# Kernel optimization log

Measured on AMD Instinct MI355X. Metric: run time of the kernel, lower is better.

## Reference

```python
import jax, jax.numpy as jnp
import numpy as np

N, I, C, P, K = 16, 4096, 16, 16, 8
NI = N * I
E_RAND = 524288
CP = C + P


def setup_inputs() -> dict:
    key = jax.random.key(0)
    ks = jax.random.split(key, 14)
    x = jax.random.normal(ks[0], (N, I, C), dtype=jnp.float32)
    # random edges (stand-in for data-dependent kmeans complete subgraphs) + self loops
    src = jax.random.randint(ks[1], (E_RAND,), 0, NI)
    dst = jax.random.randint(ks[2], (E_RAND,), 0, NI)
    loops = jnp.arange(NI)
    edge_index = jnp.stack([jnp.concatenate([src, loops]),
                            jnp.concatenate([dst, loops])], axis=0)  # [2, E]
    # cluster labels: point p of cloud n -> cluster (p % K) + n*K, every cluster non-empty
    cluster_index = (jnp.arange(NI) % K) + (jnp.arange(NI) // I) * K
    sC = 1.0 / np.sqrt(C)
    sCP = 1.0 / np.sqrt(CP)
    return {
        "x": x,
        "edge_index": edge_index,
        "cluster_index": cluster_index,
        "F_W": jax.random.normal(ks[3], (C, C * CP), dtype=jnp.float32) * sC,
        "F_b": jnp.zeros((C * CP,), dtype=jnp.float32),
        "W_W": jax.random.normal(ks[4], (C, C * CP), dtype=jnp.float32) * sC,
        "W_b": jnp.zeros((C * CP,), dtype=jnp.float32),
        "M_W": jax.random.normal(ks[5], (CP, 1), dtype=jnp.float32) * sCP,
        "M_b": jnp.zeros((1,), dtype=jnp.float32),
        "B": jax.random.normal(ks[6], (CP,), dtype=jnp.float32),
        "mlp1_W": jax.random.normal(ks[7], (CP, CP), dtype=jnp.float32) * sCP,
        "mlp1_b": jnp.zeros((CP,), dtype=jnp.float32),
        "mlp2_W": jax.random.normal(ks[8], (CP, CP), dtype=jnp.float32) * sCP,
        "mlp2_b": jnp.zeros((CP,), dtype=jnp.float32),
        "sc_W": jax.random.normal(ks[9], (CP, CP), dtype=jnp.float32) * sCP,
        "sc_b": jnp.zeros((CP,), dtype=jnp.float32),
        "lr": jnp.asarray(1.0, dtype=jnp.float32),
    }


def _shrinking_unit(x, edge_index, cluster_index,
                    F_W, F_b, W_W, W_b, M_W, M_b, B,
                    mlp1_W, mlp1_b, mlp2_W, mlp2_b, sc_W, sc_b, lr):
    xf = x.reshape(-1, C)                      # [NI, C]
    src, dst = edge_index[0], edge_index[1]    # message flows src(j) -> dst(i)
    x_i = xf[dst]                              # [E, C]
    x_j = xf[src]
    # message: per-edge transform matrix F(x_j - x_i) in R^{(C+P) x C} applied to x_i
    msg = ((x_j - x_i) @ F_W + F_b).reshape(-1, CP, C)   # [E, CP, C]
    msg = jnp.einsum('epc,ec->ep', msg, x_i)             # [E, CP]
    # mean aggregation over incoming edges (self-loops guarantee deg >= 1)
    deg = jax.ops.segment_sum(jnp.ones_like(dst, dtype=x.dtype), dst, num_segments=NI)
    aggr = jax.ops.segment_sum(msg, dst, num_segments=NI) / deg[:, None]   # [NI, CP]
    # update
    weight = aggr @ M_W + M_b                             # [NI, 1]
    aggr = aggr * weight
    transform = (xf @ W_W + W_b).reshape(-1, CP, C)       # [NI, CP, C]
    aggr = aggr + jnp.einsum('npc,nc->np', transform, xf)
    conv = jax.nn.sigmoid(aggr + B).reshape(N, I, CP)     # [N, I, CP]
    # Aggregation module: pad x to CP, squeeze-excite style softmax gate
    x_pad = jnp.pad(x, ((0, 0), (0, 0), (0, P)))          # [N, I, CP]
    S1 = jnp.mean(x_pad, axis=1)                          # [N, CP]
    S2 = jnp.mean(conv, axis=1)
    Z1 = S1 @ mlp1_W + mlp1_b
    Z2 = S2 @ mlp2_W + mlp2_b
    M = jax.nn.softmax(jnp.stack([Z1, Z2], axis=0), axis=0)  # [2, N, CP]
    fused = M[0][:, None, :] * x_pad + M[1][:, None, :] * conv  # [N, I, CP]
    # MaxPool over clusters
    pooled = jax.ops.segment_max(fused.reshape(-1, CP), cluster_index,
                                 num_segments=K * N).reshape(N, K, CP)
    # SelfCorrelation: residual MLP scaled by learnable lambda
    pf = pooled.reshape(-1, CP)
    out = (pf + lr * (pf @ sc_W + sc_b)).reshape(N, K, CP)
    return out


def reference(x, edge_index, cluster_index, F_W, F_b, W_W, W_b, M_W, M_b, B,
              mlp1_W, mlp1_b, mlp2_W, mlp2_b, sc_W, sc_b, lr):
    return _shrinking_unit(x, edge_index, cluster_index, F_W, F_b, W_W, W_b,
                           M_W, M_b, B, mlp1_W, mlp1_b, mlp2_W, mlp2_b,
                           sc_W, sc_b, lr)
```

## Files before the change

### kernel.cpp

```cpp
#include <hip/hip_runtime.h>
#include <hip/hip_bf16.h>


#define POOL_NBLK 32

__device__ __forceinline__ unsigned fmap(float f) {
    unsigned u = __float_as_uint(f);
    return (u & 0x80000000u) ? ~u : (u | 0x80000000u);
}
__device__ __forceinline__ float funmap(unsigned m) {
    return (m & 0x80000000u) ? __uint_as_float(m & 0x7FFFFFFFu)
                             : __uint_as_float(~m);
}

__device__ __forceinline__ void load16(const float* __restrict__ p, float* r) {
    const float4* q = (const float4*)p;
    float4 a = q[0], b = q[1], c = q[2], d = q[3];
    r[0]=a.x; r[1]=a.y; r[2]=a.z; r[3]=a.w;
    r[4]=b.x; r[5]=b.y; r[6]=b.z; r[7]=b.w;
    r[8]=c.x; r[9]=c.y; r[10]=c.z; r[11]=c.w;
    r[12]=d.x; r[13]=d.y; r[14]=d.z; r[15]=d.w;
}

__global__ __launch_bounds__(256) void edge_scatter(
    const float* __restrict__ x, const int* __restrict__ ei,
    float* __restrict__ s, float* __restrict__ deg, int E)
{
    int tid = blockIdx.x * 256 + threadIdx.x;
    int e = tid >> 4, c = tid & 15;
    if (e >= E) return;
    int src = ei[e];
    int dst = ei[E + e];
    atomicAdd(&s[(size_t)dst * 16 + c], x[(size_t)src * 16 + c]);
    if (c == 0) atomicAdd(&deg[dst], 1.0f);
}

__global__ __launch_bounds__(256) void node_update(
    const float* __restrict__ x, const float* __restrict__ s,
    const float* __restrict__ deg,
    const float* __restrict__ Fw, const float* __restrict__ Fb,
    const float* __restrict__ Ww, const float* __restrict__ Wb,
    const float* __restrict__ Mw, const float* __restrict__ Mb,
    const float* __restrict__ Bv,
    float* __restrict__ conv, float* __restrict__ S1s, float* __restrict__ S2s)
{
    __shared__ float wlds[8192];
    __shared__ float aF[256 * 17];
    const int tid = threadIdx.x;
    #pragma unroll
    for (int k = 0; k < 8192; k += 256) wlds[k + tid] = Fw[k + tid];

    const int lane = tid & 63;
    const int w4   = tid >> 6;
    const int h    = w4 & 1;
    const int i    = blockIdx.x * 128 + ((w4 >> 1) << 6) + lane;
    const int n    = i >> 12;

    float xr[16], tr[16];
    load16(x + (size_t)i * 16, xr);
    load16(s + (size_t)i * 16, tr);
    const float invd = 1.0f / deg[i];
    #pragma unroll
    for (int c = 0; c < 16; ++c) tr[c] = tr[c] * invd - xr[c];

    __syncthreads();

    const int pbase = h << 8;
    #pragma unroll 1
    for (int pp = 0; pp < 16; ++pp) {
        const int cb0 = pbase + (pp << 4);
        float acc = 0.0f;
        #pragma unroll
        for (int cb = 0; cb < 16; cb += 4) {
            float u0 = Fb[cb0+cb+0], u1 = Fb[cb0+cb+1];
            float u2 = Fb[cb0+cb+2], u3 = Fb[cb0+cb+3];
            #pragma unroll
            for (int cp = 0; cp < 16; ++cp) {
                const float4 f = *(const float4*)&wlds[(cp << 9) + cb0 + cb];
                u0 = fmaf(tr[cp], f.x, u0);
                u1 = fmaf(tr[cp], f.y, u1);
                u2 = fmaf(tr[cp], f.z, u2);
                u3 = fmaf(tr[cp], f.w, u3);
            }
            acc = fmaf(xr[cb+0], u0, acc);
            acc = fmaf(xr[cb+1], u1, acc);
            acc = fmaf(xr[cb+2], u2, acc);
            acc = fmaf(xr[cb+3], u3, acc);
        }
        aF[tid * 17 + pp] = acc;
    }
    __syncthreads();
    #pragma unroll
    for (int k = 0; k < 8192; k += 256) wlds[k + tid] = Ww[k + tid];

    float w = Mb[0];
    {
        const int base0 = (tid & ~64) * 17;
        const int base1 = base0 + 64 * 17;
        #pragma unroll
        for (int q = 0; q < 16; ++q) w = fmaf(aF[base0 + q], Mw[q], w);
        #pragma unroll
        for (int q = 0; q < 16; ++q) w = fmaf(aF[base1 + q], Mw[16 + q], w);
    }
    __syncthreads();

    #pragma unroll 1
    for (int pp = 0; pp < 16; ++pp) {
        const int cb0 = pbase + (pp << 4);
        float acc = 0.0f;
        #pragma unroll
        for (int cb = 0; cb < 16; cb += 4) {
            float u0 = Wb[cb0+cb+0], u1 = Wb[cb0+cb+1];
            float u2 = Wb[cb0+cb+2], u3 = Wb[cb0+cb+3];
            #pragma unroll
            for (int cp = 0; cp < 16; ++cp) {
                const float4 f = *(const float4*)&wlds[(cp << 9) + cb0 + cb];
                u0 = fmaf(xr[cp], f.x, u0);
                u1 = fmaf(xr[cp], f.y, u1);
                u2 = fmaf(xr[cp], f.z, u2);
                u3 = fmaf(xr[cp], f.w, u3);
            }
            acc = fmaf(xr[cb+0], u0, acc);
            acc = fmaf(xr[cb+1], u1, acc);
            acc = fmaf(xr[cb+2], u2, acc);
            acc = fmaf(xr[cb+3], u3, acc);
        }
        const float z  = aF[tid * 17 + pp] * w + acc + Bv[(h << 4) + pp];
        const float cv = 1.0f / (1.0f + expf(-z));
        conv[(size_t)i * 32 + (h << 4) + pp] = cv;
        float v = cv;
        v += __shfl_xor(v, 1);
        v += __shfl_xor(v, 2);
        v += __shfl_xor(v, 4);
        v += __shfl_xor(v, 8);
        v += __shfl_xor(v, 16);
        v += __shfl_xor(v, 32);
        if (lane == 0) atomicAdd(&S2s[n * 32 + (h << 4) + pp], v);
    }
    if (h == 0) {
        #pragma unroll
        for (int c = 0; c < 16; ++c) {
            float v = xr[c];
            v += __shfl_xor(v, 1);
            v += __shfl_xor(v, 2);
            v += __shfl_xor(v, 4);
            v += __shfl_xor(v, 8);
            v += __shfl_xor(v, 16);
            v += __shfl_xor(v, 32);
            if (lane == 0) atomicAdd(&S1s[n * 32 + c], v);
        }
    }
}

__global__ void gate_kernel(const float* __restrict__ S1s, const float* __restrict__ S2s,
    const float* __restrict__ m1W, const float* __restrict__ m1b,
    const float* __restrict__ m2W, const float* __restrict__ m2b,
    float* __restrict__ M0, float* __restrict__ M1, float invI)
{
    int t = threadIdx.x;
    int n = t >> 5, p = t & 31;
    float z1 = m1b[p], z2 = m2b[p];
    #pragma unroll
    for (int q = 0; q < 32; ++q) {
        z1 = fmaf(S1s[n * 32 + q] * invI, m1W[q * 32 + p], z1);
        z2 = fmaf(S2s[n * 32 + q] * invI, m2W[q * 32 + p], z2);
    }
    float m = fmaxf(z1, z2);
    float e1 = expf(z1 - m), e2 = expf(z2 - m);
    float inv = 1.0f / (e1 + e2);
    M0[t] = e1 * inv;
    M1[t] = e2 * inv;
}

__global__ __launch_bounds__(256) void pool_kernel(
    const float* __restrict__ x, const float* __restrict__ conv,
    const int* __restrict__ cl, const float* __restrict__ M0,
    const float* __restrict__ M1, unsigned* __restrict__ blkT,
    int NI, int nSlots)
{
    __shared__ unsigned utab[4096];
    const int tid = threadIdx.x;
    for (int t = tid; t < nSlots; t += 256) utab[t] = 0u;
    __syncthreads();

    for (int i = blockIdx.x * 256 + tid; i < NI; i += POOL_NBLK * 256) {
        int n = i >> 12;
        int c = cl[i];
        const float* m0 = M0 + n * 32;
        const float* m1 = M1 + n * 32;
        float cr[32];
        {
            const float4* q = (const float4*)(conv + (size_t)i * 32);
            #pragma unroll
            for (int b = 0; b < 8; ++b) {
                float4 v = q[b];
                cr[b*4+0] = v.x; cr[b*4+1] = v.y; cr[b*4+2] = v.z; cr[b*4+3] = v.w;
            }
        }
        float xr[16];
        load16(x + (size_t)i * 16, xr);
        unsigned* up = utab + (c << 5);
        #pragma unroll
        for (int p = 0; p < 16; ++p) {
            float f = fmaf(m0[p], xr[p], m1[p] * cr[p]);
            atomicMax(&up[p], fmap(f));
        }
        #pragma unroll
        for (int p = 16; p < 32; ++p) {
            float f = m1[p] * cr[p];
            atomicMax(&up[p], fmap(f));
        }
    }
    __syncthreads();
    unsigned* dst = blkT + (size_t)blockIdx.x * nSlots;
    for (int t = tid; t < nSlots; t += 256) dst[t] = utab[t];
}

__global__ __launch_bounds__(256) void pool_reduce(
    const unsigned* __restrict__ blkT, unsigned* __restrict__ pooledM, int nSlots)
{
    int t = blockIdx.x * 256 + threadIdx.x;
    if (t >= nSlots) return;
    unsigned m = 0u;
    #pragma unroll
    for (int b = 0; b < POOL_NBLK; ++b)
        m = max(m, blkT[(size_t)b * nSlots + t]);
    pooledM[t] = m;
}

__global__ void final_kernel(const unsigned* __restrict__ pooledM,
    const float* __restrict__ scW, const float* __restrict__ scb,
    const float* __restrict__ lr, float* __restrict__ out, int total)
{
    int t = blockIdx.x * 256 + threadIdx.x;
    if (t >= total) return;
    int g = t >> 5, p = t & 31;
    float acc = scb[p];
    float self = 0.0f;
    #pragma unroll
    for (int q = 0; q < 32; ++q) {
        float v = funmap(pooledM[g * 32 + q]);
        if (q == p) self = v;
        acc = fmaf(v, scW[q * 32 + p], acc);
    }
    out[t] = self + lr[0] * acc;
}

extern "C" void kernel_launch(void* const* d_in, const int* in_sizes, int n_in,
                              void* d_out, int out_size, void* d_ws, size_t ws_size,
                              hipStream_t stream)
{
    const float* x   = (const float*)d_in[0];
    const int*   ei  = (const int*)d_in[1];
    const int*   clus= (const int*)d_in[2];
    const float* Fw  = (const float*)d_in[3];
    const float* Fb  = (const float*)d_in[4];
    const float* Ww  = (const float*)d_in[5];
    const float* Wb  = (const float*)d_in[6];
    const float* Mw  = (const float*)d_in[7];
    const float* Mb  = (const float*)d_in[8];
    const float* Bv  = (const float*)d_in[9];
    const float* m1W = (const float*)d_in[10];
    const float* m1b = (const float*)d_in[11];
    const float* m2W = (const float*)d_in[12];
    const float* m2b = (const float*)d_in[13];
    const float* scW = (const float*)d_in[14];
    const float* scb = (const float*)d_in[15];
    const float* lr  = (const float*)d_in[16];

    const int NI = in_sizes[0] / 16;
    const int E  = in_sizes[1] / 2;
    const int nG = NI >> 12;
    const int nC = out_size / 32;
    const int nSlots = nC * 32;

    float* ws   = (float*)d_ws;
    float* s_   = ws;
    float* deg_ = s_ + (size_t)NI * 16;
    float* S1s  = deg_ + NI;
    float* S2s  = S1s + nG * 32;
    unsigned* pooledM = (unsigned*)(S2s + nG * 32);
    float* M0   = (float*)(pooledM + nSlots);
    float* M1   = M0 + nG * 32;
    float* conv = M1 + nG * 32;
    unsigned* blkT = (unsigned*)s_;

    size_t need_bytes = (size_t)((char*)(conv + (size_t)NI * 32) - (char*)ws);
    if (ws_size < need_bytes || nSlots > 4096) return;

    size_t zbytes = (size_t)((char*)(pooledM + nSlots) - (char*)ws);
    hipMemsetAsync(d_ws, 0, zbytes, stream);

    edge_scatter<<<dim3((E * 16 + 255) / 256), dim3(256), 0, stream>>>(x, ei, s_, deg_, E);
    node_update<<<dim3(NI * 2 / 256), dim3(256), 0, stream>>>(
        x, s_, deg_, Fw, Fb, Ww, Wb, Mw, Mb, Bv, conv, S1s, S2s);
    gate_kernel<<<dim3(1), dim3(nG * 32), 0, stream>>>(
        S1s, S2s, m1W, m1b, m2W, m2b, M0, M1, 1.0f / 4096.0f);
    pool_kernel<<<dim3(POOL_NBLK), dim3(256), 0, stream>>>(
        x, conv, clus, M0, M1, blkT, NI, nSlots);
    pool_reduce<<<dim3((nSlots + 255) / 256), dim3(256), 0, stream>>>(
        blkT, pooledM, nSlots);
    final_kernel<<<dim3((out_size + 255) / 256), dim3(256), 0, stream>>>(
        pooledM, scW, scb, lr, (float*)d_out, out_size);
}
```

Baseline: 276.8 us.

## Process two nodes per thread in node_update and widen pool block count

```diff
diff --git a/kernel.cpp b/kernel.cpp
--- a/kernel.cpp
+++ b/kernel.cpp
@@ -2,7 +2,7 @@
 #include <hip/hip_bf16.h>
 
 
-#define POOL_NBLK 32
+#define POOL_NBLK 256
 
 __device__ __forceinline__ unsigned fmap(float f) {
     unsigned u = __float_as_uint(f);
@@ -35,7 +35,7 @@
     if (c == 0) atomicAdd(&deg[dst], 1.0f);
 }
 
-__global__ __launch_bounds__(256) void node_update(
+__global__ __launch_bounds__(128) void node_update(
     const float* __restrict__ x, const float* __restrict__ s,
     const float* __restrict__ deg,
     const float* __restrict__ Fw, const float* __restrict__ Fb,
@@ -45,23 +45,34 @@
     float* __restrict__ conv, float* __restrict__ S1s, float* __restrict__ S2s)
 {
     __shared__ float wlds[8192];
-    __shared__ float aF[256 * 17];
+    __shared__ float aF[128 * 34];
     const int tid = threadIdx.x;
+
+    {
+        const float4* F4 = (const float4*)Fw;
+        float4* w4 = (float4*)wlds;
+        #pragma unroll
+        for (int k = 0; k < 16; ++k) w4[k * 128 + tid] = F4[k * 128 + tid];
+    }
+
+    const int lane = tid & 63;
+    const int h    = tid >> 6;
+    const int i0   = blockIdx.x * 128 + lane;
+    const int i1   = i0 + 64;
+    const int n    = i0 >> 12;
+
+    float xr0[16], tr0[16], xr1[16], tr1[16];
+    load16(x + (size_t)i0 * 16, xr0);
+    load16(s + (size_t)i0 * 16, tr0);
+    load16(x + (size_t)i1 * 16, xr1);
+    load16(s + (size_t)i1 * 16, tr1);
+    const float invd0 = 1.0f / deg[i0];
+    const float invd1 = 1.0f / deg[i1];
     #pragma unroll
-    for (int k = 0; k < 8192; k += 256) wlds[k + tid] = Fw[k + tid];
-
-    const int lane = tid & 63;
-    const int w4   = tid >> 6;
-    const int h    = w4 & 1;
-    const int i    = blockIdx.x * 128 + ((w4 >> 1) << 6) + lane;
-    const int n    = i >> 12;
-
-    float xr[16], tr[16];
-    load16(x + (size_t)i * 16, xr);
-    load16(s + (size_t)i * 16, tr);
-    const float invd = 1.0f / deg[i];
-    #pragma unroll
-    for (int c = 0; c < 16; ++c) tr[c] = tr[c] * invd - xr[c];
+    for (int c = 0; c < 16; ++c) {
+        tr0[c] = tr0[c] * invd0 - xr0[c];
+        tr1[c] = tr1[c] * invd1 - xr1[c];
+    }
 
     __syncthreads();
 
@@ -69,66 +80,98 @@
     #pragma unroll 1
     for (int pp = 0; pp < 16; ++pp) {
         const int cb0 = pbase + (pp << 4);
-        float acc = 0.0f;
+        float acc0 = 0.0f, acc1 = 0.0f;
         #pragma unroll
         for (int cb = 0; cb < 16; cb += 4) {
-            float u0 = Fb[cb0+cb+0], u1 = Fb[cb0+cb+1];
-            float u2 = Fb[cb0+cb+2], u3 = Fb[cb0+cb+3];
+            const float b0 = Fb[cb0+cb+0], b1 = Fb[cb0+cb+1];
+            const float b2 = Fb[cb0+cb+2], b3 = Fb[cb0+cb+3];
+            float u00=b0,u01=b1,u02=b2,u03=b3;
+            float u10=b0,u11=b1,u12=b2,u13=b3;
             #pragma unroll
             for (int cp = 0; cp < 16; ++cp) {
                 const float4 f = *(const float4*)&wlds[(cp << 9) + cb0 + cb];
-                u0 = fmaf(tr[cp], f.x, u0);
-                u1 = fmaf(tr[cp], f.y, u1);
-                u2 = fmaf(tr[cp], f.z, u2);
-                u3 = fmaf(tr[cp], f.w, u3);
+                u00 = fmaf(tr0[cp], f.x, u00);
+                u01 = fmaf(tr0[cp], f.y, u01);
+                u02 = fmaf(tr0[cp], f.z, u02);
+                u03 = fmaf(tr0[cp], f.w, u03);
+                u10 = fmaf(tr1[cp], f.x, u10);
+                u11 = fmaf(tr1[cp], f.y, u11);
+                u12 = fmaf(tr1[cp], f.z, u12);
+                u13 = fmaf(tr1[cp], f.w, u13);
             }
-            acc = fmaf(xr[cb+0], u0, acc);
-            acc = fmaf(xr[cb+1], u1, acc);
-            acc = fmaf(xr[cb+2], u2, acc);
-            acc = fmaf(xr[cb+3], u3, acc);
-        }
-        aF[tid * 17 + pp] = acc;
-    }
-    __syncthreads();
-    #pragma unroll
-    for (int k = 0; k < 8192; k += 256) wlds[k + tid] = Ww[k + tid];
-
-    float w = Mb[0];
+            acc0 = fmaf(xr0[cb+0], u00, acc0);
+            acc0 = fmaf(xr0[cb+1], u01, acc0);
+            acc0 = fmaf(xr0[cb+2], u02, acc0);
+            acc0 = fmaf(xr0[cb+3], u03, acc0);
+            acc1 = fmaf(xr1[cb+0], u10, acc1);
+            acc1 = fmaf(xr1[cb+1], u11, acc1);
+            acc1 = fmaf(xr1[cb+2], u12, acc1);
+            acc1 = fmaf(xr1[cb+3], u13, acc1);
+        }
+        aF[tid * 34 + pp]      = acc0;
+        aF[tid * 34 + 17 + pp] = acc1;
+    }
+    __syncthreads();
     {
-        const int base0 = (tid & ~64) * 17;
-        const int base1 = base0 + 64 * 17;
-        #pragma unroll
-        for (int q = 0; q < 16; ++q) w = fmaf(aF[base0 + q], Mw[q], w);
-        #pragma unroll
-        for (int q = 0; q < 16; ++q) w = fmaf(aF[base1 + q], Mw[16 + q], w);
+        const float4* W4 = (const float4*)Ww;
+        float4* w4 = (float4*)wlds;
+        #pragma unroll
+        for (int k = 0; k < 16; ++k) w4[k * 128 + tid] = W4[k * 128 + tid];
+    }
+
+    float wgt0 = Mb[0], wgt1 = Mb[0];
+    {
+        const int r0 = lane * 34;
+        const int r1 = (64 + lane) * 34;
+        #pragma unroll
+        for (int q = 0; q < 16; ++q) {
+            wgt0 = fmaf(aF[r0 + q],      Mw[q],      wgt0);
+            wgt0 = fmaf(aF[r1 + q],      Mw[16 + q], wgt0);
+            wgt1 = fmaf(aF[r0 + 17 + q], Mw[q],      wgt1);
+            wgt1 = fmaf(aF[r1 + 17 + q], Mw[16 + q], wgt1);
+        }
     }
     __syncthreads();
 
     #pragma unroll 1
     for (int pp = 0; pp < 16; ++pp) {
         const int cb0 = pbase + (pp << 4);
-        float acc = 0.0f;
+        float acc0 = 0.0f, acc1 = 0.0f;
         #pragma unroll
         for (int cb = 0; cb < 16; cb += 4) {
-            float u0 = Wb[cb0+cb+0], u1 = Wb[cb0+cb+1];
-            float u2 = Wb[cb0+cb+2], u3 = Wb[cb0+cb+3];
+            const float b0 = Wb[cb0+cb+0], b1 = Wb[cb0+cb+1];
+            const float b2 = Wb[cb0+cb+2], b3 = Wb[cb0+cb+3];
+            float u00=b0,u01=b1,u02=b2,u03=b3;
+            float u10=b0,u11=b1,u12=b2,u13=b3;
             #pragma unroll
             for (int cp = 0; cp < 16; ++cp) {
                 const float4 f = *(const float4*)&wlds[(cp << 9) + cb0 + cb];
-                u0 = fmaf(xr[cp], f.x, u0);
-                u1 = fmaf(xr[cp], f.y, u1);
-                u2 = fmaf(xr[cp], f.z, u2);
-                u3 = fmaf(xr[cp], f.w, u3);
+                u00 = fmaf(xr0[cp], f.x, u00);
+                u01 = fmaf(xr0[cp], f.y, u01);
+                u02 = fmaf(xr0[cp], f.z, u02);
+                u03 = fmaf(xr0[cp], f.w, u03);
+                u10 = fmaf(xr1[cp], f.x, u10);
+                u11 = fmaf(xr1[cp], f.y, u11);
+                u12 = fmaf(xr1[cp], f.z, u12);
+                u13 = fmaf(xr1[cp], f.w, u13);
             }
-            acc = fmaf(xr[cb+0], u0, acc);
-            acc = fmaf(xr[cb+1], u1, acc);
-            acc = fmaf(xr[cb+2], u2, acc);
-            acc = fmaf(xr[cb+3], u3, acc);
-        }
-        const float z  = aF[tid * 17 + pp] * w + acc + Bv[(h << 4) + pp];
-        const float cv = 1.0f / (1.0f + expf(-z));
-        conv[(size_t)i * 32 + (h << 4) + pp] = cv;
-        float v = cv;
+            acc0 = fmaf(xr0[cb+0], u00, acc0);
+            acc0 = fmaf(xr0[cb+1], u01, acc0);
+            acc0 = fmaf(xr0[cb+2], u02, acc0);
+            acc0 = fmaf(xr0[cb+3], u03, acc0);
+            acc1 = fmaf(xr1[cb+0], u10, acc1);
+            acc1 = fmaf(xr1[cb+1], u11, acc1);
+            acc1 = fmaf(xr1[cb+2], u12, acc1);
+            acc1 = fmaf(xr1[cb+3], u13, acc1);
+        }
+        const float bv = Bv[(h << 4) + pp];
+        const float z0 = aF[tid * 34 + pp]      * wgt0 + acc0 + bv;
+        const float z1 = aF[tid * 34 + 17 + pp] * wgt1 + acc1 + bv;
+        const float cv0 = 1.0f / (1.0f + expf(-z0));
+        const float cv1 = 1.0f / (1.0f + expf(-z1));
+        conv[(size_t)i0 * 32 + (h << 4) + pp] = cv0;
+        conv[(size_t)i1 * 32 + (h << 4) + pp] = cv1;
+        float v = cv0 + cv1;
         v += __shfl_xor(v, 1);
         v += __shfl_xor(v, 2);
         v += __shfl_xor(v, 4);
@@ -140,7 +183,7 @@
     if (h == 0) {
         #pragma unroll
         for (int c = 0; c < 16; ++c) {
-            float v = xr[c];
+            float v = xr0[c] + xr1[c];
             v += __shfl_xor(v, 1);
             v += __shfl_xor(v, 2);
             v += __shfl_xor(v, 4);
@@ -222,7 +265,7 @@
     int t = blockIdx.x * 256 + threadIdx.x;
     if (t >= nSlots) return;
     unsigned m = 0u;
-    #pragma unroll
+    #pragma unroll 8
     for (int b = 0; b < POOL_NBLK; ++b)
         m = max(m, blkT[(size_t)b * nSlots + t]);
     pooledM[t] = m;
@@ -287,12 +330,13 @@
 
     size_t need_bytes = (size_t)((char*)(conv + (size_t)NI * 32) - (char*)ws);
     if (ws_size < need_bytes || nSlots > 4096) return;
+    if ((size_t)POOL_NBLK * nSlots > (size_t)NI * 16) return;
 
     size_t zbytes = (size_t)((char*)(pooledM + nSlots) - (char*)ws);
     hipMemsetAsync(d_ws, 0, zbytes, stream);
 
     edge_scatter<<<dim3((E * 16 + 255) / 256), dim3(256), 0, stream>>>(x, ei, s_, deg_, E);
-    node_update<<<dim3(NI * 2 / 256), dim3(256), 0, stream>>>(
+    node_update<<<dim3(NI / 128), dim3(128), 0, stream>>>(
         x, s_, deg_, Fw, Fb, Ww, Wb, Mw, Mb, Bv, conv, S1s, S2s);
     gate_kernel<<<dim3(1), dim3(nG * 32), 0, stream>>>(
         S1s, S2s, m1W, m1b, m2W, m2b, M0, M1, 1.0f / 4096.0f);
```

New measurement: 268.6 us. 3.0% less time.
